# Kernel tuning notes

Measured on AMD Instinct MI355X. Metric: run time of the kernel, lower is better.

## Reference

```python
import jax, jax.numpy as jnp
import numpy as np

N_COARSE = 24
N_FINE = 1000
TOTAL_NODES = N_COARSE + N_FINE  # 1024
BATCH = 32768


def _build_state_space():
    # Faithful port of generateStateSpace for levels==2.
    # hierarchy: fine node (N_COARSE + i) has parent coarse node (i % N_COARSE),
    # fine nodes visited in order so every coarse row is inserted on first sight.
    S = np.zeros((TOTAL_NODES + 1, TOTAL_NODES), dtype=np.float32)
    recorded = np.zeros(TOTAL_NODES, dtype=np.int64)
    i = 1
    for f in range(N_FINE):
        fine = N_COARSE + f
        coarse = f % N_COARSE
        if recorded[coarse] == 0:
            S[i, coarse] = 1.0
            recorded[coarse] = 1
            i += 1
        S[i, coarse] = 1.0
        S[i, fine] = 1.0
        i += 1
    assert i == TOTAL_NODES + 1, 'Invalid StateSpace'
    return jnp.asarray(S)


def setup_inputs() -> dict:
    key = jax.random.key(0)
    k_fs, k_lab = jax.random.split(key)
    fs = jax.random.normal(k_fs, (BATCH, TOTAL_NODES), dtype=jnp.float32)
    labels = jax.random.randint(k_lab, (BATCH,), 0, TOTAL_NODES)
    stateSpace = _build_state_space()  # [TOTAL_NODES+1, TOTAL_NODES]
    return {'fs': fs, 'labels': labels, 'stateSpace': stateSpace}


def reference(fs, labels, stateSpace):
    # joint[s, b] = exp(sum_n stateSpace[s, n] * fs[b, n])
    joint = jnp.exp(jnp.einsum('sn,bn->sb', stateSpace, fs))  # [S, B]
    z = jnp.sum(joint, axis=0)                                # [B]
    # selector: states s that contain label[b] (stateSpace[s, label_b] > 0)
    sel = stateSpace[:, labels] > 0                           # [S, B]
    marginal = jnp.sum(jnp.where(sel, joint, 0.0), axis=0)    # [B]
    loss = -(jnp.log(marginal) - jnp.log(z))                  # = -log(marginal / z)
    return jnp.mean(loss)
```

## Files before the change

### kernel.cpp

```cpp
#include <hip/hip_runtime.h>
#include <hip/hip_bf16.h>


constexpr int N_COARSE = 24;
constexpr int TOTAL = 1024;
constexpr int BATCH = 32768;
constexpr int WAVES_PER_BLOCK = 4;
constexpr int GRID1 = BATCH / WAVES_PER_BLOCK;

__global__ __launch_bounds__(256) void treeloss_partial(
    const float* __restrict__ fs, const int* __restrict__ labels,
    float* __restrict__ partials) {
  const int wave = threadIdx.x >> 6;
  const int lane = threadIdx.x & 63;
  const int b = blockIdx.x * WAVES_PER_BLOCK + wave;

  __shared__ float sc48[WAVES_PER_BLOCK][48];
  __shared__ float blocksum[WAVES_PER_BLOCK];

  const float* __restrict__ row = fs + (size_t)b * TOTAL;
  const float4* __restrict__ row4 = reinterpret_cast<const float4*>(row);
  const int label = labels[b];

  const float4 v0 = row4[lane];
  const float4 v1 = row4[lane + 64];
  const float4 v2 = row4[lane + 128];
  const float4 v3 = row4[lane + 192];

  if (lane < N_COARSE) {
    const float e = __expf(row[lane]);
    sc48[wave][lane] = e;
    sc48[wave][lane + N_COARSE] = e;
  }
  __syncthreads();

  const int cbase = (lane * 4) % N_COARSE;
  float zp = 0.0f;

  {
    const float vv[4] = {v0.x, v0.y, v0.z, v0.w};
#pragma unroll
    for (int k = 0; k < 4; ++k) {
      const int n = lane * 4 + k;
      const float en = __expf(vv[k]);
      if (n < N_COARSE) zp += en;
      else zp += sc48[wave][cbase + k] * en;
    }
  }
  {
    const float vv[4] = {v1.x, v1.y, v1.z, v1.w};
#pragma unroll
    for (int k = 0; k < 4; ++k)
      zp += sc48[wave][cbase + 16 + k] * __expf(vv[k]);
  }
  {
    const float vv[4] = {v2.x, v2.y, v2.z, v2.w};
#pragma unroll
    for (int k = 0; k < 4; ++k)
      zp += sc48[wave][cbase + 8 + k] * __expf(vv[k]);
  }
  {
    const float vv[4] = {v3.x, v3.y, v3.z, v3.w};
#pragma unroll
    for (int k = 0; k < 4; ++k)
      zp += sc48[wave][cbase + k] * __expf(vv[k]);
  }

  float g = 0.0f;
  if (label < N_COARSE) {
    const int idx = label + N_COARSE * (lane + 1);
    if (idx < TOTAL) g = __expf(row[idx]);
  }

#pragma unroll
  for (int off = 32; off > 0; off >>= 1) {
    zp += __shfl_down(zp, off);
    g += __shfl_down(g, off);
  }

  if (lane == 0) {
    float m;
    if (label < N_COARSE) m = sc48[wave][label] * (1.0f + g);
    else m = sc48[wave][label % N_COARSE] * __expf(row[label]);
    blocksum[wave] = __logf(1.0f + zp) - __logf(m);
  }
  __syncthreads();

  if (threadIdx.x == 0) {
    partials[blockIdx.x] = blocksum[0] + blocksum[1] + blocksum[2] + blocksum[3];
  }
}

__global__ __launch_bounds__(1024) void treeloss_reduce(
    const float* __restrict__ partials, float* __restrict__ out) {
  const int tid = threadIdx.x;
  const int lane = tid & 63;
  const int wave = tid >> 6;
  const float4* __restrict__ p4 = reinterpret_cast<const float4*>(partials);
  const float4 a = p4[tid];
  const float4 c = p4[tid + 1024];
  float s = (a.x + a.y + a.z + a.w) + (c.x + c.y + c.z + c.w);
#pragma unroll
  for (int off = 32; off > 0; off >>= 1) s += __shfl_down(s, off);
  __shared__ float ps[16];
  if (lane == 0) ps[wave] = s;
  __syncthreads();
  if (tid == 0) {
    float t = 0.0f;
#pragma unroll
    for (int w = 0; w < 16; ++w) t += ps[w];
    out[0] = t * (1.0f / (float)BATCH);
  }
}

extern "C" void kernel_launch(void* const* d_in, const int* in_sizes, int n_in,
                              void* d_out, int out_size, void* d_ws, size_t ws_size,
                              hipStream_t stream) {
  const float* fs = (const float*)d_in[0];
  const int* labels = (const int*)d_in[1];
  float* out = (float*)d_out;
  float* partials = (float*)d_ws;

  treeloss_partial<<<GRID1, 256, 0, stream>>>(fs, labels, partials);
  treeloss_reduce<<<1, 1024, 0, stream>>>(partials, out);
}
```

Baseline: 189.8 us.

## Process multiple rows per wave with double-buffered loads and shuffle-based coarse broadcast

Switches the partial kernel to a persistent style where each wave handles several rows (1024 blocks × 4 waves, 8 rows each). The next row's data is prefetched into registers while the current one is computed. The shared-memory coarse-exp table and the block syncs are replaced by wave shuffles, and there are fewer partials for the reduce kernel to read. This is meant to hide load latency and cut launch, scheduling and LDS/barrier overhead, at the cost of more registers and fewer waves in flight.

```diff
diff --git a/kernel.cpp b/kernel.cpp
--- a/kernel.cpp
+++ b/kernel.cpp
@@ -5,110 +5,125 @@
 constexpr int N_COARSE = 24;
 constexpr int TOTAL = 1024;
 constexpr int BATCH = 32768;
-constexpr int WAVES_PER_BLOCK = 4;
-constexpr int GRID1 = BATCH / WAVES_PER_BLOCK;
+constexpr int WPB = 4;
+constexpr int GRID1 = 1024;
+constexpr int NWAVES = GRID1 * WPB;
+constexpr int RPW = BATCH / NWAVES;
 
 __global__ __launch_bounds__(256) void treeloss_partial(
     const float* __restrict__ fs, const int* __restrict__ labels,
     float* __restrict__ partials) {
   const int wave = threadIdx.x >> 6;
   const int lane = threadIdx.x & 63;
-  const int b = blockIdx.x * WAVES_PER_BLOCK + wave;
-
-  __shared__ float sc48[WAVES_PER_BLOCK][48];
-  __shared__ float blocksum[WAVES_PER_BLOCK];
-
-  const float* __restrict__ row = fs + (size_t)b * TOTAL;
-  const float4* __restrict__ row4 = reinterpret_cast<const float4*>(row);
-  const int label = labels[b];
-
-  const float4 v0 = row4[lane];
-  const float4 v1 = row4[lane + 64];
-  const float4 v2 = row4[lane + 128];
-  const float4 v3 = row4[lane + 192];
-
-  if (lane < N_COARSE) {
-    const float e = __expf(row[lane]);
-    sc48[wave][lane] = e;
-    sc48[wave][lane + N_COARSE] = e;
-  }
-  __syncthreads();
+  const int w = blockIdx.x * WPB + wave;
+  const int b0 = w * RPW;
 
   const int cbase = (lane * 4) % N_COARSE;
-  float zp = 0.0f;
+  int idx1[4], idx2[4];
+#pragma unroll
+  for (int k = 0; k < 4; ++k) {
+    const int t1 = cbase + 16 + k; idx1[k] = (t1 >= N_COARSE) ? t1 - N_COARSE : t1;
+    const int t2 = cbase + 8 + k;  idx2[k] = (t2 >= N_COARSE) ? t2 - N_COARSE : t2;
+  }
+
+  float4 buf[2][4];
+  float  cbuf[2];
+  int    lbuf[2];
 
   {
-    const float vv[4] = {v0.x, v0.y, v0.z, v0.w};
-#pragma unroll
-    for (int k = 0; k < 4; ++k) {
-      const int n = lane * 4 + k;
-      const float en = __expf(vv[k]);
-      if (n < N_COARSE) zp += en;
-      else zp += sc48[wave][cbase + k] * en;
-    }
-  }
-  {
-    const float vv[4] = {v1.x, v1.y, v1.z, v1.w};
-#pragma unroll
-    for (int k = 0; k < 4; ++k)
-      zp += sc48[wave][cbase + 16 + k] * __expf(vv[k]);
-  }
-  {
-    const float vv[4] = {v2.x, v2.y, v2.z, v2.w};
-#pragma unroll
-    for (int k = 0; k < 4; ++k)
-      zp += sc48[wave][cbase + 8 + k] * __expf(vv[k]);
-  }
-  {
-    const float vv[4] = {v3.x, v3.y, v3.z, v3.w};
-#pragma unroll
-    for (int k = 0; k < 4; ++k)
-      zp += sc48[wave][cbase + k] * __expf(vv[k]);
+    const float* r = fs + (size_t)b0 * TOTAL;
+    const float4* r4 = reinterpret_cast<const float4*>(r);
+    buf[0][0] = r4[lane];       buf[0][1] = r4[lane + 64];
+    buf[0][2] = r4[lane + 128]; buf[0][3] = r4[lane + 192];
+    cbuf[0] = (lane < N_COARSE) ? r[lane] : 0.0f;
+    lbuf[0] = labels[b0];
   }
 
-  float g = 0.0f;
-  if (label < N_COARSE) {
-    const int idx = label + N_COARSE * (lane + 1);
-    if (idx < TOTAL) g = __expf(row[idx]);
+  float loss = 0.0f;
+#pragma unroll
+  for (int rr = 0; rr < RPW; ++rr) {
+    const int cur = rr & 1, nxt = cur ^ 1;
+    if (rr + 1 < RPW) {
+      const float* r = fs + (size_t)(b0 + rr + 1) * TOTAL;
+      const float4* r4 = reinterpret_cast<const float4*>(r);
+      buf[nxt][0] = r4[lane];       buf[nxt][1] = r4[lane + 64];
+      buf[nxt][2] = r4[lane + 128]; buf[nxt][3] = r4[lane + 192];
+      cbuf[nxt] = (lane < N_COARSE) ? r[lane] : 0.0f;
+      lbuf[nxt] = labels[b0 + rr + 1];
+    }
+
+    const float ec = __expf(cbuf[cur]);
+    const int label = lbuf[cur];
+    const float* row = fs + (size_t)(b0 + rr) * TOTAL;
+
+    float zp = 0.0f;
+    {
+      const float4 v = buf[cur][0];
+      const float vv[4] = {v.x, v.y, v.z, v.w};
+#pragma unroll
+      for (int k = 0; k < 4; ++k) {
+        float mult = __shfl(ec, cbase + k);
+        if (lane < 6) mult = 1.0f;
+        zp += mult * __expf(vv[k]);
+      }
+    }
+    {
+      const float4 v = buf[cur][1];
+      const float vv[4] = {v.x, v.y, v.z, v.w};
+#pragma unroll
+      for (int k = 0; k < 4; ++k) zp += __shfl(ec, idx1[k]) * __expf(vv[k]);
+    }
+    {
+      const float4 v = buf[cur][2];
+      const float vv[4] = {v.x, v.y, v.z, v.w};
+#pragma unroll
+      for (int k = 0; k < 4; ++k) zp += __shfl(ec, idx2[k]) * __expf(vv[k]);
+    }
+    {
+      const float4 v = buf[cur][3];
+      const float vv[4] = {v.x, v.y, v.z, v.w};
+#pragma unroll
+      for (int k = 0; k < 4; ++k) zp += __shfl(ec, cbase + k) * __expf(vv[k]);
+    }
+
+    float g = 0.0f;
+    const bool coarse_label = (label < N_COARSE);
+    if (coarse_label) {
+      const int gi = label + N_COARSE * (lane + 1);
+      if (gi < TOTAL) g = __expf(row[gi]);
+    }
+
+#pragma unroll
+    for (int off = 32; off > 0; off >>= 1) {
+      zp += __shfl_xor(zp, off);
+      g  += __shfl_xor(g, off);
+    }
+
+    const int c_eff = coarse_label ? label : (label % N_COARSE);
+    const float el = __shfl(ec, c_eff);
+    const float m = coarse_label ? el * (1.0f + g) : el * __expf(row[label]);
+    loss += __logf(1.0f + zp) - __logf(m);
   }
 
-#pragma unroll
-  for (int off = 32; off > 0; off >>= 1) {
-    zp += __shfl_down(zp, off);
-    g += __shfl_down(g, off);
-  }
-
-  if (lane == 0) {
-    float m;
-    if (label < N_COARSE) m = sc48[wave][label] * (1.0f + g);
-    else m = sc48[wave][label % N_COARSE] * __expf(row[label]);
-    blocksum[wave] = __logf(1.0f + zp) - __logf(m);
-  }
-  __syncthreads();
-
-  if (threadIdx.x == 0) {
-    partials[blockIdx.x] = blocksum[0] + blocksum[1] + blocksum[2] + blocksum[3];
-  }
+  if (lane == 0) partials[w] = loss;
 }
 
 __global__ __launch_bounds__(1024) void treeloss_reduce(
     const float* __restrict__ partials, float* __restrict__ out) {
   const int tid = threadIdx.x;
   const int lane = tid & 63;
-  const int wave = tid >> 6;
-  const float4* __restrict__ p4 = reinterpret_cast<const float4*>(partials);
-  const float4 a = p4[tid];
-  const float4 c = p4[tid + 1024];
-  float s = (a.x + a.y + a.z + a.w) + (c.x + c.y + c.z + c.w);
+  const int wv = tid >> 6;
+  const float4 a = reinterpret_cast<const float4*>(partials)[tid];
+  float s = (a.x + a.y) + (a.z + a.w);
 #pragma unroll
-  for (int off = 32; off > 0; off >>= 1) s += __shfl_down(s, off);
+  for (int off = 32; off > 0; off >>= 1) s += __shfl_xor(s, off);
   __shared__ float ps[16];
-  if (lane == 0) ps[wave] = s;
+  if (lane == 0) ps[wv] = s;
   __syncthreads();
   if (tid == 0) {
     float t = 0.0f;
 #pragma unroll
-    for (int w = 0; w < 16; ++w) t += ps[w];
+    for (int k = 0; k < 16; ++k) t += ps[k];
     out[0] = t * (1.0f / (float)BATCH);
   }
 }
```

After: 195.6 us. +3.0%, slower.

## Process two rows per wave and replace LDS coarse table with shuffles

Applied to the files above, without the earlier changes.

Each wave now handles two batch rows, issuing eight float4 loads up front to raise memory-level parallelism. The shared-memory coarse exp table and block barriers are replaced by cross-lane shuffles of the coarse exponentials. Each wave writes its own partial, so the reduce kernel sums twice as many partials. This costs more registers per wave and more shuffle instructions, and the kernel stays bound by HBM bandwidth on a 128MB read.

```diff
diff --git a/kernel.cpp b/kernel.cpp
--- a/kernel.cpp
+++ b/kernel.cpp
@@ -5,89 +5,115 @@
 constexpr int N_COARSE = 24;
 constexpr int TOTAL = 1024;
 constexpr int BATCH = 32768;
-constexpr int WAVES_PER_BLOCK = 4;
-constexpr int GRID1 = BATCH / WAVES_PER_BLOCK;
+constexpr int RPW = 2;
+constexpr int NWAVES = BATCH / RPW;
+constexpr int TPB = 256;
+constexpr int GRID1 = NWAVES / (TPB / 64);
 
-__global__ __launch_bounds__(256) void treeloss_partial(
+__global__ __launch_bounds__(TPB, 4) void treeloss_partial(
     const float* __restrict__ fs, const int* __restrict__ labels,
     float* __restrict__ partials) {
   const int wave = threadIdx.x >> 6;
   const int lane = threadIdx.x & 63;
-  const int b = blockIdx.x * WAVES_PER_BLOCK + wave;
+  const int w = blockIdx.x * (TPB / 64) + wave;
+  const int b0 = w * RPW;
 
-  __shared__ float sc48[WAVES_PER_BLOCK][48];
-  __shared__ float blocksum[WAVES_PER_BLOCK];
+  const float* __restrict__ rowA = fs + (size_t)b0 * TOTAL;
+  const float* __restrict__ rowB = rowA + TOTAL;
+  const float4* __restrict__ a4 = reinterpret_cast<const float4*>(rowA);
+  const float4* __restrict__ c4 = reinterpret_cast<const float4*>(rowB);
 
-  const float* __restrict__ row = fs + (size_t)b * TOTAL;
-  const float4* __restrict__ row4 = reinterpret_cast<const float4*>(row);
-  const int label = labels[b];
-
-  const float4 v0 = row4[lane];
-  const float4 v1 = row4[lane + 64];
-  const float4 v2 = row4[lane + 128];
-  const float4 v3 = row4[lane + 192];
-
-  if (lane < N_COARSE) {
-    const float e = __expf(row[lane]);
-    sc48[wave][lane] = e;
-    sc48[wave][lane + N_COARSE] = e;
-  }
-  __syncthreads();
+  const float4 a0 = a4[lane], a1 = a4[lane + 64], a2 = a4[lane + 128], a3 = a4[lane + 192];
+  const float4 b0v = c4[lane], b1 = c4[lane + 64], b2 = c4[lane + 128], b3 = c4[lane + 192];
+  const float cA = (lane < N_COARSE) ? rowA[lane] : 0.0f;
+  const float cB = (lane < N_COARSE) ? rowB[lane] : 0.0f;
+  const int labA = labels[b0];
+  const int labB = labels[b0 + 1];
+  const float lvA = rowA[labA];
+  const float lvB = rowB[labB];
 
   const int cbase = (lane * 4) % N_COARSE;
-  float zp = 0.0f;
+  int i1[4], i2[4];
+#pragma unroll
+  for (int k = 0; k < 4; ++k) {
+    const int t1 = cbase + 16 + k; i1[k] = (t1 >= N_COARSE) ? t1 - N_COARSE : t1;
+    const int t2 = cbase + 8 + k;  i2[k] = (t2 >= N_COARSE) ? t2 - N_COARSE : t2;
+  }
 
+  const float ecA = __expf(cA);
+  const float ecB = __expf(cB);
+
+  float zpA = 0.0f, zpB = 0.0f;
   {
-    const float vv[4] = {v0.x, v0.y, v0.z, v0.w};
+    const float avv[4] = {a0.x, a0.y, a0.z, a0.w};
+    const float bvv[4] = {b0v.x, b0v.y, b0v.z, b0v.w};
 #pragma unroll
     for (int k = 0; k < 4; ++k) {
-      const int n = lane * 4 + k;
-      const float en = __expf(vv[k]);
-      if (n < N_COARSE) zp += en;
-      else zp += sc48[wave][cbase + k] * en;
+      float mA = __shfl(ecA, cbase + k), mB = __shfl(ecB, cbase + k);
+      if (lane < 6) { mA = 1.0f; mB = 1.0f; }
+      zpA += mA * __expf(avv[k]);
+      zpB += mB * __expf(bvv[k]);
     }
   }
   {
-    const float vv[4] = {v1.x, v1.y, v1.z, v1.w};
+    const float avv[4] = {a1.x, a1.y, a1.z, a1.w};
+    const float bvv[4] = {b1.x, b1.y, b1.z, b1.w};
 #pragma unroll
-    for (int k = 0; k < 4; ++k)
-      zp += sc48[wave][cbase + 16 + k] * __expf(vv[k]);
+    for (int k = 0; k < 4; ++k) {
+      zpA += __shfl(ecA, i1[k]) * __expf(avv[k]);
+      zpB += __shfl(ecB, i1[k]) * __expf(bvv[k]);
+    }
   }
   {
-    const float vv[4] = {v2.x, v2.y, v2.z, v2.w};
+    const float avv[4] = {a2.x, a2.y, a2.z, a2.w};
+    const float bvv[4] = {b2.x, b2.y, b2.z, b2.w};
 #pragma unroll
-    for (int k = 0; k < 4; ++k)
-      zp += sc48[wave][cbase + 8 + k] * __expf(vv[k]);
+    for (int k = 0; k < 4; ++k) {
+      zpA += __shfl(ecA, i2[k]) * __expf(avv[k]);
+      zpB += __shfl(ecB, i2[k]) * __expf(bvv[k]);
+    }
   }
   {
-    const float vv[4] = {v3.x, v3.y, v3.z, v3.w};
+    const float avv[4] = {a3.x, a3.y, a3.z, a3.w};
+    const float bvv[4] = {b3.x, b3.y, b3.z, b3.w};
 #pragma unroll
-    for (int k = 0; k < 4; ++k)
-      zp += sc48[wave][cbase + k] * __expf(vv[k]);
-  }
-
-  float g = 0.0f;
-  if (label < N_COARSE) {
-    const int idx = label + N_COARSE * (lane + 1);
-    if (idx < TOTAL) g = __expf(row[idx]);
+    for (int k = 0; k < 4; ++k) {
+      zpA += __shfl(ecA, cbase + k) * __expf(avv[k]);
+      zpB += __shfl(ecB, cbase + k) * __expf(bvv[k]);
+    }
   }
 
 #pragma unroll
   for (int off = 32; off > 0; off >>= 1) {
-    zp += __shfl_down(zp, off);
-    g += __shfl_down(g, off);
+    zpA += __shfl_xor(zpA, off);
+    zpB += __shfl_xor(zpB, off);
+  }
+
+  float mA, mB;
+  if (labA < N_COARSE) {
+    float g = 0.0f;
+    const int gi = labA + N_COARSE * (lane + 1);
+    if (gi < TOTAL) g = __expf(rowA[gi]);
+#pragma unroll
+    for (int off = 32; off > 0; off >>= 1) g += __shfl_xor(g, off);
+    mA = __shfl(ecA, labA) * (1.0f + g);
+  } else {
+    mA = __shfl(ecA, labA % N_COARSE) * __expf(lvA);
+  }
+  if (labB < N_COARSE) {
+    float g = 0.0f;
+    const int gi = labB + N_COARSE * (lane + 1);
+    if (gi < TOTAL) g = __expf(rowB[gi]);
+#pragma unroll
+    for (int off = 32; off > 0; off >>= 1) g += __shfl_xor(g, off);
+    mB = __shfl(ecB, labB) * (1.0f + g);
+  } else {
+    mB = __shfl(ecB, labB % N_COARSE) * __expf(lvB);
   }
 
   if (lane == 0) {
-    float m;
-    if (label < N_COARSE) m = sc48[wave][label] * (1.0f + g);
-    else m = sc48[wave][label % N_COARSE] * __expf(row[label]);
-    blocksum[wave] = __logf(1.0f + zp) - __logf(m);
-  }
-  __syncthreads();
-
-  if (threadIdx.x == 0) {
-    partials[blockIdx.x] = blocksum[0] + blocksum[1] + blocksum[2] + blocksum[3];
+    partials[w] = (__logf(1.0f + zpA) - __logf(mA)) +
+                  (__logf(1.0f + zpB) - __logf(mB));
   }
 }
 
@@ -95,20 +121,23 @@
     const float* __restrict__ partials, float* __restrict__ out) {
   const int tid = threadIdx.x;
   const int lane = tid & 63;
-  const int wave = tid >> 6;
+  const int wv = tid >> 6;
   const float4* __restrict__ p4 = reinterpret_cast<const float4*>(partials);
-  const float4 a = p4[tid];
-  const float4 c = p4[tid + 1024];
-  float s = (a.x + a.y + a.z + a.w) + (c.x + c.y + c.z + c.w);
+  float s = 0.0f;
 #pragma unroll
-  for (int off = 32; off > 0; off >>= 1) s += __shfl_down(s, off);
+  for (int i = 0; i < NWAVES / 4 / 1024; ++i) {
+    const float4 a = p4[tid + i * 1024];
+    s += (a.x + a.y) + (a.z + a.w);
+  }
+#pragma unroll
+  for (int off = 32; off > 0; off >>= 1) s += __shfl_xor(s, off);
   __shared__ float ps[16];
-  if (lane == 0) ps[wave] = s;
+  if (lane == 0) ps[wv] = s;
   __syncthreads();
   if (tid == 0) {
     float t = 0.0f;
 #pragma unroll
-    for (int w = 0; w < 16; ++w) t += ps[w];
+    for (int k = 0; k < 16; ++k) t += ps[k];
     out[0] = t * (1.0f / (float)BATCH);
   }
 }
@@ -121,6 +150,6 @@
   float* out = (float*)d_out;
   float* partials = (float*)d_ws;
 
-  treeloss_partial<<<GRID1, 256, 0, stream>>>(fs, labels, partials);
+  treeloss_partial<<<GRID1, TPB, 0, stream>>>(fs, labels, partials);
   treeloss_reduce<<<1, 1024, 0, stream>>>(partials, out);
 }
```

After: 193.8 us. 1.02x slower.
